# Kernel optimization log

Measured on AMD Instinct MI355X. Metric: run time of the kernel, lower is better.

The kernel has to match this reference:

```python
import jax, jax.numpy as jnp
import numpy as np

H, D, DIM = 8, 128, 1024   # heads, dim_head, model dim (inner_dim = H*D = DIM)
QB, N = 16, 512            # 'q' and 'n' dims of the [q, n, dim] inputs


def layer_norm(x, g, b, eps=1e-5):
    mu = x.mean(-1, keepdims=True)
    var = ((x - mu) ** 2).mean(-1, keepdims=True)
    return (x - mu) / jnp.sqrt(var + eps) * g + b


def setup_inputs() -> dict:
    key = jax.random.key(0)
    ks = jax.random.split(key, 8)
    rn = lambda k, shape, s=1.0: jax.random.normal(k, shape, jnp.float32) * s
    return {
        'q': rn(ks[0], (QB, N, DIM)),
        'k': rn(ks[1], (QB, N, DIM)),
        'v': rn(ks[2], (QB, N, DIM)),
        'ln_g': jnp.ones(DIM, jnp.float32),
        'ln_b': jnp.zeros(DIM, jnp.float32),
        'w_in': rn(ks[3], (H * D, DIM), 0.02),          # Linear(dim -> inner_dim), no bias
        'wp_w1': rn(ks[4], (D, 2 * D), 0.05),           # weight_predictor Linear(2d -> d)
        'wp_b1': jnp.zeros(D, jnp.float32),
        'wp_ln_g': jnp.ones(D, jnp.float32),
        'wp_ln_b': jnp.zeros(D, jnp.float32),
        'wp_w2': rn(ks[5], (3, D), 0.05),               # Linear(d -> 3)
        'wp_b2': jnp.zeros(3, jnp.float32),
        'w_out': rn(ks[6], (DIM, H * D), 0.02),         # output Linear(inner_dim -> dim)
        'b_out': jnp.zeros(DIM, jnp.float32),
    }


def reference(q, k, v, ln_g, ln_b, w_in, wp_w1, wp_b1, wp_ln_g, wp_ln_b,
              wp_w2, wp_b2, w_out, b_out):
    def proj(t):
        x = layer_norm(t, ln_g, ln_b) @ w_in.T                 # [Q, N, H*D]
        Qd, Nd = t.shape[0], t.shape[1]
        return x.reshape(Qd, Nd, H, D).transpose(2, 0, 1, 3)   # [h, q, n, d]

    f_q, f_k, f_v = proj(q), proj(k), proj(v)

    # cosine similarity component
    dots = jnp.einsum('hqnd,hqmd->hqnm', f_q, f_k)
    qn = jnp.linalg.norm(f_q, axis=-1)                          # [h, q, n]
    kn = jnp.linalg.norm(f_k, axis=-1)                          # [h, q, m]
    cosine_sim = dots / (qn[..., :, None] * kn[..., None, :])

    q_centered = f_q - f_q.mean(-1, keepdims=True)

    # variance component (unbiased variance, clipped ratio vs target_var=1)
    q_var = jnp.var(f_q, axis=-1, ddof=1)
    k_var = jnp.var(f_k, axis=-1, ddof=1)
    q_ratio = 2.0 * jnp.minimum(q_var, 1.0) / (q_var + 1.0)
    k_ratio = 2.0 * jnp.minimum(k_var, 1.0) / (k_var + 1.0)
    var_component = jnp.einsum('hqn,hqm->hqnm', q_ratio, k_ratio)

    # decorrelation-scaled covariance component (overwrites the dead loop in the source)
    q_flat = q_centered.reshape(H, -1, D)                        # [h, q*n, d]
    feat_corr = jnp.einsum('hnd,hne->hde', q_flat, q_flat) / q_flat.shape[1]
    feat_corr = feat_corr * (1.0 - jnp.eye(D, dtype=feat_corr.dtype))
    decorr_score = jnp.linalg.norm(feat_corr, axis=(-2, -1)) / (D * D)
    decorr_scale = jnp.exp(-5.0 * decorr_score)[:, None, None, None]
    cov_component = cosine_sim * decorr_scale

    # dynamic per-head weight mixing
    q_global = f_q.mean(axis=(1, 2))                             # [h, d]
    k_global = f_k.mean(axis=(1, 2))
    feats = jnp.concatenate([q_global, k_global], axis=-1)       # [h, 2d]
    h1 = jnp.maximum(layer_norm(feats @ wp_w1.T + wp_b1, wp_ln_g, wp_ln_b), 0.0)
    weights = jax.nn.softmax(h1 @ wp_w2.T + wp_b2, axis=-1)      # [h, 3]
    cw = weights[:, 0][:, None, None, None]
    vw = weights[:, 1][:, None, None, None]
    ww = weights[:, 2][:, None, None, None]
    mixed = cw * cosine_sim + vw * cov_component + ww * var_component

    out = jnp.einsum('hqnm,hqmd->hqnd', mixed, f_v)
    out = out.transpose(1, 2, 0, 3).reshape(q.shape[0], q.shape[1], H * D)
    return out @ w_out.T + b_out
```

## Files before the change

kernel.cpp:

```cpp
#include <hip/hip_runtime.h>
#include <hip/hip_bf16.h>

typedef unsigned short u16;
typedef __attribute__((ext_vector_type(8))) short short8;
typedef __attribute__((ext_vector_type(4))) float floatx4;

#define H 8
#define D 128
#define DIM 1024
#define QB 16
#define NSEQ 512
#define R 8192

__device__ inline u16 f2b(float x) {
    union { float f; unsigned int u; } c{x};
    unsigned int lsb = (c.u >> 16) & 1;
    unsigned int r = c.u + 0x7fffu + lsb;
    return (u16)(r >> 16);
}
__device__ inline float b2f(u16 u) {
    union { unsigned int i; float f; } c;
    c.i = (unsigned int)u << 16;
    return c.f;
}

#define GLOAD_LDS16(gptr, lptr)                                                        \
    __builtin_amdgcn_global_load_lds(                                                  \
        (const __attribute__((address_space(1))) unsigned int*)(gptr),                 \
        (__attribute__((address_space(3))) unsigned int*)(lptr), 16, 0, 0)

__global__ __launch_bounds__(256) void prep(const float* __restrict__ q,
                                            const float* __restrict__ k,
                                            const float* __restrict__ v,
                                            const float* __restrict__ g,
                                            const float* __restrict__ b,
                                            u16* __restrict__ out,
                                            const float* __restrict__ w_in,
                                            const float* __restrict__ w_out,
                                            u16* __restrict__ w_in16,
                                            u16* __restrict__ w_out16) {
    const int bb = blockIdx.x;
    const int tid = threadIdx.x;
    if (bb < 2048) {
        const int n4each = DIM * DIM / 4;
        int i = bb * 256 + tid;
        const float* src; u16* dst; int j;
        if (i < n4each) { src = w_in;  dst = w_in16;  j = i; }
        else            { src = w_out; dst = w_out16; j = i - n4each; }
        float4 vv = *(const float4*)(src + (size_t)j * 4);
        ushort4 pk;
        pk.x = f2b(vv.x); pk.y = f2b(vv.y); pk.z = f2b(vv.z); pk.w = f2b(vv.w);
        *(ushort4*)(dst + (size_t)j * 4) = pk;
        return;
    }
    const int b2 = bb - 2048;
    const int wv = tid >> 6, lane = tid & 63;
    const int row = b2 * 4 + wv;
    const int y = row >> 13, r = row & 8191;
    const float* src = (y == 0) ? q : (y == 1) ? k : v;
    const float* rp = src + (size_t)r * DIM;
    float4 x0 = *(const float4*)(rp + (0 * 64 + lane) * 4);
    float4 x1 = *(const float4*)(rp + (1 * 64 + lane) * 4);
    float4 x2 = *(const float4*)(rp + (2 * 64 + lane) * 4);
    float4 x3 = *(const float4*)(rp + (3 * 64 + lane) * 4);
    float sum = (x0.x + x0.y + x0.z + x0.w) + (x1.x + x1.y + x1.z + x1.w)
              + (x2.x + x2.y + x2.z + x2.w) + (x3.x + x3.y + x3.z + x3.w);
    float sq = x0.x*x0.x + x0.y*x0.y + x0.z*x0.z + x0.w*x0.w
             + x1.x*x1.x + x1.y*x1.y + x1.z*x1.z + x1.w*x1.w
             + x2.x*x2.x + x2.y*x2.y + x2.z*x2.z + x2.w*x2.w
             + x3.x*x3.x + x3.y*x3.y + x3.z*x3.z + x3.w*x3.w;
#pragma unroll
    for (int o = 32; o > 0; o >>= 1) {
        sum += __shfl_xor(sum, o);
        sq  += __shfl_xor(sq, o);
    }
    float mean = sum * (1.0f / DIM);
    float var = sq * (1.0f / DIM) - mean * mean;
    float rstd = rsqrtf(var + 1e-5f);
    u16* op = out + ((size_t)y * R + r) * DIM;
    float4 xs[4] = {x0, x1, x2, x3};
#pragma unroll
    for (int p = 0; p < 4; p++) {
        int e4 = (p * 64 + lane) * 4;
        float4 gv = *(const float4*)(g + e4);
        float4 bv = *(const float4*)(b + e4);
        ushort4 pk;
        pk.x = f2b((xs[p].x - mean) * rstd * gv.x + bv.x);
        pk.y = f2b((xs[p].y - mean) * rstd * gv.y + bv.y);
        pk.z = f2b((xs[p].z - mean) * rstd * gv.z + bv.z);
        pk.w = f2b((xs[p].w - mean) * rstd * gv.w + bv.w);
        *(ushort4*)(op + e4) = pk;
    }
}

__global__ __launch_bounds__(256) void gemm_qkv(const u16* __restrict__ A,
                                                const u16* __restrict__ B,
                                                u16* __restrict__ qT,
                                                u16* __restrict__ fqb,
                                                u16* __restrict__ kTh,
                                                u16* __restrict__ vT,
                                                float* __restrict__ qn,
                                                float* __restrict__ qm,
                                                float* __restrict__ qr,
                                                float* __restrict__ kn,
                                                float* __restrict__ kr) {
    __shared__ __align__(16) u16 smem[19712];
    u16* As  = smem;
    u16* Bs  = smem + 4096;
    u16* As2 = smem + 8192;
    u16* Bs2 = smem + 12288;
    float* sred = (float*)(smem + 18432);
    float* invb = (float*)(smem + 19456);

    const int tid = threadIdx.x;
    const int bb = blockIdx.x;
    const int xcd = bb & 7, j0 = bb >> 3;
    const int h = j0 & 7;
    const int rowblk = xcd * 24 + (j0 >> 3);
    const int m0 = rowblk * 128, n0 = h * 128;
    const int seg = rowblk >> 6;
    const int lrb = (rowblk & 63) * 128;

    const int wave = tid >> 6, lane = tid & 63;
    const int wm = (wave >> 1) * 64, wn = (wave & 1) * 64;
    const int fr = lane & 15, kq = lane >> 4;
    const int srow = tid >> 2, scol = (tid & 3) * 8;

    floatx4 acc[4][4] = {};
    const size_t aOff0 = (size_t)(m0 + srow) * DIM + scol;
    const size_t aOff1 = (size_t)(m0 + 64 + srow) * DIM + scol;
    const size_t bOff0 = (size_t)(n0 + srow) * DIM + scol;
    const size_t bOff1 = (size_t)(n0 + 64 + srow) * DIM + scol;

    for (int kt = 0; kt < DIM; kt += 64) {
        GLOAD_LDS16(A + aOff0 + kt, As + tid * 8);
        GLOAD_LDS16(A + aOff1 + kt, As + (256 + tid) * 8);
        GLOAD_LDS16(B + bOff0 + kt, Bs + tid * 8);
        GLOAD_LDS16(B + bOff1 + kt, Bs + (256 + tid) * 8);
        GLOAD_LDS16(A + aOff0 + kt + 32, As2 + tid * 8);
        GLOAD_LDS16(A + aOff1 + kt + 32, As2 + (256 + tid) * 8);
        GLOAD_LDS16(B + bOff0 + kt + 32, Bs2 + tid * 8);
        GLOAD_LDS16(B + bOff1 + kt + 32, Bs2 + (256 + tid) * 8);
        __syncthreads();
        short8 xf[4], wf[4];
#pragma unroll
        for (int i = 0; i < 4; i++)
            xf[i] = *(const short8*)&As[(wm + i * 16 + fr) * 32 + kq * 8];
#pragma unroll
        for (int j = 0; j < 4; j++)
            wf[j] = *(const short8*)&Bs[(wn + j * 16 + fr) * 32 + kq * 8];
#pragma unroll
        for (int j = 0; j < 4; j++)
#pragma unroll
            for (int i = 0; i < 4; i++)
                acc[j][i] = __builtin_amdgcn_mfma_f32_16x16x32_bf16(wf[j], xf[i], acc[j][i], 0, 0, 0);
        short8 xg[4], wg[4];
#pragma unroll
        for (int i = 0; i < 4; i++)
            xg[i] = *(const short8*)&As2[(wm + i * 16 + fr) * 32 + kq * 8];
#pragma unroll
        for (int j = 0; j < 4; j++)
            wg[j] = *(const short8*)&Bs2[(wn + j * 16 + fr) * 32 + kq * 8];
#pragma unroll
        for (int j = 0; j < 4; j++)
#pragma unroll
            for (int i = 0; i < 4; i++)
                acc[j][i] = __builtin_amdgcn_mfma_f32_16x16x32_bf16(wg[j], xg[i], acc[j][i], 0, 0, 0);
        __syncthreads();
    }

    if (seg <= 1) {
        const int half = wn >> 6;
#pragma unroll
        for (int i = 0; i < 4; i++) {
            float s = 0.0f, qs = 0.0f;
#pragma unroll
            for (int j = 0; j < 4; j++)
#pragma unroll
                for (int rg = 0; rg < 4; rg++) {
                    float vv = acc[j][i][rg];
                    s += vv; qs += vv * vv;
                }
            s += __shfl_xor(s, 16); qs += __shfl_xor(qs, 16);
            s += __shfl_xor(s, 32); qs += __shfl_xor(qs, 32);
            if (kq == 0) {
                int rl = wm + i * 16 + fr;
                sred[rl * 4 + half * 2 + 0] = s;
                sred[rl * 4 + half * 2 + 1] = qs;
            }
        }
        __syncthreads();
        if (tid < 128) {
            float sum = sred[tid * 4 + 0] + sred[tid * 4 + 2];
            float sq  = sred[tid * 4 + 1] + sred[tid * 4 + 3];
            float nrm = sqrtf(sq);
            float var = (sq - sum * sum * (1.0f / D)) * (1.0f / (D - 1));
            float ratio = 2.0f * fminf(var, 1.0f) / (var + 1.0f);
            size_t idx = (size_t)h * R + lrb + tid;
            if (seg == 0) {
                qn[idx] = nrm; qm[idx] = sum * (1.0f / D); qr[idx] = ratio;
            } else {
                kn[idx] = nrm; kr[idx] = ratio;
                invb[tid] = 1.0f / nrm;
            }
        }
        __syncthreads();
    }

    u16* dstT = (seg == 0) ? qT : (seg == 1) ? kTh : vT;
#pragma unroll
    for (int i = 0; i < 4; i++) {
        const int rl = wm + i * 16 + fr;
        const float sc = (seg == 1) ? invb[rl] : 1.0f;
#pragma unroll
        for (int j = 0; j < 4; j++) {
#pragma unroll
            for (int rg = 0; rg < 4; rg++) {
                const int cl = wn + j * 16 + kq * 4 + rg;
                dstT[(size_t)(h * D + cl) * R + lrb + rl] = f2b(acc[j][i][rg] * sc);
            }
        }
    }

    if (seg == 0) {
        __syncthreads();
        u16* Tw = smem + wave * 4608;
#pragma unroll
        for (int i = 0; i < 4; i++)
#pragma unroll
            for (int j = 0; j < 4; j++) {
                ushort4 pk;
                pk.x = f2b(acc[j][i][0]); pk.y = f2b(acc[j][i][1]);
                pk.z = f2b(acc[j][i][2]); pk.w = f2b(acc[j][i][3]);
                *(ushort4*)&Tw[(i * 16 + fr) * 72 + j * 16 + kq * 4] = pk;
            }
        __syncthreads();
#pragma unroll
        for (int p = 0; p < 16; p++) {
            int rloc = p * 4 + kq;
            int c4 = fr * 4;
            ushort4 v = *(const ushort4*)&Tw[rloc * 72 + c4];
            *(ushort4*)&fqb[(size_t)(lrb + wm + rloc) * DIM + h * D + wn + c4] = v;
        }
    }
}

__global__ __launch_bounds__(256) void fanout(const u16* __restrict__ qT,
                                              const u16* __restrict__ kTh,
                                              const u16* __restrict__ vT,
                                              const float* __restrict__ qm,
                                              const float* __restrict__ kn,
                                              const float* __restrict__ kr,
                                              float* __restrict__ qg,
                                              float* __restrict__ kg,
                                              float* __restrict__ ubuf,
                                              float* __restrict__ s2,
                                              float* __restrict__ P,
                                              u16* __restrict__ Mt,
                                              float* __restrict__ sv) {
    __shared__ __align__(16) u16 sm[17040];
    u16* As = sm;
    u16* Bs = sm + 8192;
    float* wbuf  = (float*)(sm + 16384);
    float* svred = (float*)(sm + 16512);
    float* redS  = (float*)(sm + 17024);

    const int bb = blockIdx.x;
    const int tid = threadIdx.x;
    const int wave = tid >> 6, lane = tid & 63;
    const int wm = (wave >> 1) * 64, wn = (wave & 1) * 64;
    const int fr = lane & 15, kq = lane >> 4;
    const int srow = tid >> 2, scol = (tid & 3) * 8;

    if (bb < 128) {
        const int qi = bb & 15, h = bb >> 4;
        const int m0g = qi * 512;
        const size_t a0 = (size_t)(h * D + srow) * R + m0g + scol;
        const size_t a1 = (size_t)(h * D + 64 + srow) * R + m0g + scol;
        const int e_id = tid & 127, mb16 = (tid >> 7) * 16;
        float svacc = 0.0f;
        floatx4 acc[4][4] = {};
        for (int kt = 0; kt < 512; kt += 64) {
#pragma unroll
            for (int kc = 0; kc < 2; kc++) {
                GLOAD_LDS16(vT + a0 + kt + kc * 32, As + kc * 4096 + tid * 8);
                GLOAD_LDS16(vT + a1 + kt + kc * 32, As + kc * 4096 + (256 + tid) * 8);
                GLOAD_LDS16(kTh + a0 + kt + kc * 32, Bs + kc * 4096 + tid * 8);
                GLOAD_LDS16(kTh + a1 + kt + kc * 32, Bs + kc * 4096 + (256 + tid) * 8);
            }
            if (tid < 64) wbuf[tid] = kr[(size_t)h * R + m0g + kt + tid];
            __syncthreads();
#pragma unroll
            for (int kc = 0; kc < 2; kc++) {
                short8 af[4], bf[4];
#pragma unroll
                for (int i = 0; i < 4; i++)
                    af[i] = *(const short8*)&As[kc * 4096 + (wm + i * 16 + fr) * 32 + kq * 8];
#pragma unroll
                for (int j = 0; j < 4; j++)
                    bf[j] = *(const short8*)&Bs[kc * 4096 + (wn + j * 16 + fr) * 32 + kq * 8];
#pragma unroll
                for (int i = 0; i < 4; i++)
#pragma unroll
                    for (int j = 0; j < 4; j++)
                        acc[i][j] = __builtin_amdgcn_mfma_f32_16x16x32_bf16(af[i], bf[j], acc[i][j], 0, 0, 0);
                short8 va = *(const short8*)&As[kc * 4096 + e_id * 32 + mb16];
                short8 vb = *(const short8*)&As[kc * 4096 + e_id * 32 + mb16 + 8];
#pragma unroll
                for (int jm = 0; jm < 8; jm++)
                    svacc += b2f((u16)va[jm]) * wbuf[kc * 32 + mb16 + jm];
#pragma unroll
                for (int jm = 0; jm < 8; jm++)
                    svacc += b2f((u16)vb[jm]) * wbuf[kc * 32 + mb16 + 8 + jm];
            }
            __syncthreads();
        }
        u16* mb = Mt + (size_t)(h * QB + qi) * D * D;
#pragma unroll
        for (int i = 0; i < 4; i++) {
            int er = wm + i * 16 + kq * 4;
#pragma unroll
            for (int j = 0; j < 4; j++) {
                int dc = wn + j * 16 + fr;
#pragma unroll
                for (int r = 0; r < 4; r++)
                    mb[(size_t)(er + r) * D + dc] = f2b(acc[i][j][r]);
            }
        }
        svred[tid] = svacc;
        __syncthreads();
        if (tid < 128)
            sv[(size_t)(h * QB + qi) * D + tid] = svred[tid] + svred[tid + 128];
    } else if (bb < 192) {
        const int t = bb - 128;
        const int c = t & 7, h = t >> 3;
        floatx4 acc[4][4] = {};
        const size_t a0 = (size_t)(h * D + srow) * R + c * 1024 + scol;
        const size_t a1 = (size_t)(h * D + 64 + srow) * R + c * 1024 + scol;
        for (int kt = 0; kt < 1024; kt += 64) {
#pragma unroll
            for (int kc = 0; kc < 2; kc++) {
                GLOAD_LDS16(qT + a0 + kt + kc * 32, As + kc * 4096 + tid * 8);
                GLOAD_LDS16(qT + a1 + kt + kc * 32, As + kc * 4096 + (256 + tid) * 8);
            }
            __syncthreads();
#pragma unroll
            for (int kc = 0; kc < 2; kc++) {
                short8 af[4], bf[4];
#pragma unroll
                for (int i = 0; i < 4; i++)
                    af[i] = *(const short8*)&As[kc * 4096 + (wm + i * 16 + fr) * 32 + kq * 8];
#pragma unroll
                for (int j = 0; j < 4; j++)
                    bf[j] = *(const short8*)&As[kc * 4096 + (wn + j * 16 + fr) * 32 + kq * 8];
#pragma unroll
                for (int i = 0; i < 4; i++)
#pragma unroll
                    for (int j = 0; j < 4; j++)
                        acc[i][j] = __builtin_amdgcn_mfma_f32_16x16x32_bf16(af[i], bf[j], acc[i][j], 0, 0, 0);
            }
            __syncthreads();
        }
        float* base = P + (size_t)(h * 8 + c) * (D * D);
#pragma unroll
        for (int i = 0; i < 4; i++) {
            int dr = wm + i * 16 + kq * 4;
#pragma unroll
            for (int j = 0; j < 4; j++) {
                int ec = wn + j * 16 + fr;
                float4 f4;
                f4.x = acc[i][j][0]; f4.y = acc[i][j][1];
                f4.z = acc[i][j][2]; f4.w = acc[i][j][3];
                *(float4*)&base[(size_t)ec * D + dr] = f4;
            }
        }
    } else {
        const int t = bb - 192;
        const int dg = t & 15, h = (t >> 4) & 7, mode = t >> 7;
        const u16* fT = mode ? kTh : qT;
        const float* wvec = mode ? kn : qm;
        const int wv = tid >> 6;
        float (*red)[4] = (float(*)[4])redS;
        const float* wp = wvec + (size_t)h * R;
        for (int dd = 0; dd < 8; dd++) {
            int d = dg * 8 + dd;
            const u16* rowp = fT + (size_t)(h * D + d) * R;
            float s = 0.0f, su = 0.0f;
            for (int it = 0; it < 8; it++) {
                int r = it * 1024 + tid * 4;
                uint2 pv = *(const uint2*)(rowp + r);
                float4 w = *(const float4*)(wp + r);
                float v0 = b2f((u16)(pv.x & 0xffffu)), v1 = b2f((u16)(pv.x >> 16));
                float v2 = b2f((u16)(pv.y & 0xffffu)), v3 = b2f((u16)(pv.y >> 16));
                if (mode) s += v0 * w.x + v1 * w.y + v2 * w.z + v3 * w.w;
                else {
                    s += v0 + v1 + v2 + v3;
                    su += v0 * w.x + v1 * w.y + v2 * w.z + v3 * w.w;
                }
            }
#pragma unroll
            for (int o = 32; o > 0; o >>= 1) {
                s += __shfl_xor(s, o);
                su += __shfl_xor(su, o);
            }
            if ((tid & 63) == 0) { red[0][wv] = s; red[1][wv] = su; }
            __syncthreads();
            if (tid == 0) {
                float S  = red[0][0] + red[0][1] + red[0][2] + red[0][3];
                float SU = red[1][0] + red[1][1] + red[1][2] + red[1][3];
                if (mode) kg[h * D + d] = S * (1.0f / R);
                else { qg[h * D + d] = S * (1.0f / R); ubuf[h * D + d] = SU; }
            }
            __syncthreads();
        }
        if (!mode && dg == 0) {
            float tt = 0.0f;
            for (int it = 0; it < 8; it++) {
                float4 m4 = *(const float4*)(qm + (size_t)h * R + it * 1024 + tid * 4);
                tt += m4.x * m4.x + m4.y * m4.y + m4.z * m4.z + m4.w * m4.w;
            }
#pragma unroll
            for (int o = 32; o > 0; o >>= 1) tt += __shfl_xor(tt, o);
            if ((tid & 63) == 0) red[0][wv] = tt;
            __syncthreads();
            if (tid == 0) s2[h] = red[0][0] + red[0][1] + red[0][2] + red[0][3];
        }
    }
}

__global__ __launch_bounds__(256) void decorr_sum(const float* __restrict__ P,
                                                  const float* __restrict__ ubuf,
                                                  const float* __restrict__ s2b,
                                                  float* __restrict__ Spart) {
    int bx = blockIdx.x, h = blockIdx.y, tid = threadIdx.x;
    float s2h = s2b[h];
    float S = 0.0f;
    for (int t = 0; t < 2; t++) {
        int de = bx * 512 + t * 256 + tid;
        int dd = de >> 7, ee = de & 127;
        float g = 0.0f;
        for (int c = 0; c < 8; c++)
            g += P[(size_t)(h * 8 + c) * (D * D) + de];
        if (dd != ee) {
            float vv = (g - ubuf[h * D + dd] - ubuf[h * D + ee] + s2h) * (1.0f / R);
            S += vv * vv;
        }
    }
#pragma unroll
    for (int o = 32; o > 0; o >>= 1) S += __shfl_xor(S, o);
    __shared__ float r1[4];
    if ((tid & 63) == 0) r1[tid >> 6] = S;
    __syncthreads();
    if (tid == 0) Spart[h * 32 + bx] = r1[0] + r1[1] + r1[2] + r1[3];
}

__global__ __launch_bounds__(256) void head_kernel(const float* __restrict__ Spart,
                                                   const float* __restrict__ qg,
                                                   const float* __restrict__ kg,
                                                   const float* __restrict__ w1,
                                                   const float* __restrict__ b1,
                                                   const float* __restrict__ lng,
                                                   const float* __restrict__ lnb,
                                                   const float* __restrict__ w2,
                                                   const float* __restrict__ b2,
                                                   float* __restrict__ coef) {
    int h = blockIdx.x, tid = threadIdx.x;
    __shared__ float s1[256], s2[256], s3[256];
    __shared__ float feats[256];
    float Ssum = 0.0f;
    for (int c = 0; c < 32; c++) Ssum += Spart[h * 32 + c];
    float dscale = expf(-5.0f * sqrtf(Ssum) / (float)(D * D));
    feats[tid] = (tid < 128) ? qg[h * D + tid] : kg[h * D + tid - 128];
    __syncthreads();
    float yv = 0.0f;
    if (tid < 128) {
        float a = b1[tid];
        for (int i = 0; i < 256; i++) a = fmaf(feats[i], w1[tid * 256 + i], a);
        yv = a;
    }
    s1[tid] = (tid < 128) ? yv : 0.0f;
    s2[tid] = (tid < 128) ? yv * yv : 0.0f;
    __syncthreads();
    for (int s = 128; s > 0; s >>= 1) {
        if (tid < s) { s1[tid] += s1[tid + s]; s2[tid] += s2[tid + s]; }
        __syncthreads();
    }
    float mean = s1[0] * (1.0f / 128.0f);
    float var = s2[0] * (1.0f / 128.0f) - mean * mean;
    float rstd = rsqrtf(var + 1e-5f);
    float rel = 0.0f;
    if (tid < 128)
        rel = fmaxf((yv - mean) * rstd * lng[tid] + lnb[tid], 0.0f);
    __syncthreads();
    s1[tid] = (tid < 128) ? rel * w2[0 * 128 + tid] : 0.0f;
    s2[tid] = (tid < 128) ? rel * w2[1 * 128 + tid] : 0.0f;
    s3[tid] = (tid < 128) ? rel * w2[2 * 128 + tid] : 0.0f;
    __syncthreads();
    for (int s = 128; s > 0; s >>= 1) {
        if (tid < s) { s1[tid] += s1[tid + s]; s2[tid] += s2[tid + s]; s3[tid] += s3[tid + s]; }
        __syncthreads();
    }
    if (tid == 0) {
        float g0 = s1[0] + b2[0], g1 = s2[0] + b2[1], g2 = s3[0] + b2[2];
        float mx = fmaxf(g0, fmaxf(g1, g2));
        float e0 = expf(g0 - mx), e1 = expf(g1 - mx), e2 = expf(g2 - mx);
        float inv = 1.0f / (e0 + e1 + e2);
        coef[h * 2 + 0] = e0 * inv + e1 * inv * dscale;
        coef[h * 2 + 1] = e2 * inv;
    }
}

__global__ __launch_bounds__(256) void attn_mfma(const u16* __restrict__ fqb,
                                                 const u16* __restrict__ Mt,
                                                 const float* __restrict__ qn,
                                                 const float* __restrict__ qr,
                                                 const float* __restrict__ sv,
                                                 const float* __restrict__ coef,
                                                 u16* __restrict__ outb) {
    __shared__ u16 As[128 * 128];
    __shared__ u16 Bs[128 * 128];
    const int nb = blockIdx.x, qi = blockIdx.y, h = blockIdx.z;
    const int tid = threadIdx.x;
    const int wave = tid >> 6, lane = tid & 63;
    const int wm = (wave >> 1) * 64, wn = (wave & 1) * 64;
    const int fr = lane & 15, kq = lane >> 4;
    const int srow = tid >> 2, scol = (tid & 3) * 8;
    const int n0g = qi * 512 + nb * 128;
    const size_t a0 = (size_t)(n0g + srow) * DIM + h * D + scol;
    const size_t a1 = (size_t)(n0g + 64 + srow) * DIM + h * D + scol;
    const u16* mtb = Mt + (size_t)(h * QB + qi) * D * D;
#pragma unroll
    for (int kc = 0; kc < 4; kc++) {
        GLOAD_LDS16(fqb + a0 + kc * 32, As + kc * 4096 + tid * 8);
        GLOAD_LDS16(fqb + a1 + kc * 32, As + kc * 4096 + (256 + tid) * 8);
        GLOAD_LDS16(mtb + (size_t)srow * D + kc * 32 + scol, Bs + kc * 4096 + tid * 8);
        GLOAD_LDS16(mtb + (size_t)(64 + srow) * D + kc * 32 + scol, Bs + kc * 4096 + (256 + tid) * 8);
    }
    __syncthreads();
    floatx4 acc[4][4] = {};
#pragma unroll
    for (int kc = 0; kc < 4; kc++) {
        short8 af[4], bf[4];
#pragma unroll
        for (int i = 0; i < 4; i++)
            af[i] = *(const short8*)&As[kc * 4096 + (wm + i * 16 + fr) * 32 + kq * 8];
#pragma unroll
        for (int j = 0; j < 4; j++)
            bf[j] = *(const short8*)&Bs[kc * 4096 + (wn + j * 16 + fr) * 32 + kq * 8];
#pragma unroll
        for (int i = 0; i < 4; i++)
#pragma unroll
            for (int j = 0; j < 4; j++)
                acc[i][j] = __builtin_amdgcn_mfma_f32_16x16x32_bf16(af[i], bf[j], acc[i][j], 0, 0, 0);
    }
    float c0 = coef[2 * h], c1 = coef[2 * h + 1];
#pragma unroll
    for (int i = 0; i < 4; i++) {
        int nr = n0g + wm + i * 16 + kq * 4;
        float4 nv = *(const float4*)&qn[(size_t)h * R + nr];
        float4 rv = *(const float4*)&qr[(size_t)h * R + nr];
        float sc1[4] = {c0 / nv.x, c0 / nv.y, c0 / nv.z, c0 / nv.w};
        float sc2[4] = {c1 * rv.x, c1 * rv.y, c1 * rv.z, c1 * rv.w};
#pragma unroll
        for (int j = 0; j < 4; j++) {
            int ec = wn + j * 16 + fr;
            float svv = sv[(size_t)(h * QB + qi) * D + ec];
#pragma unroll
            for (int r = 0; r < 4; r++)
                outb[(size_t)(nr + r) * DIM + h * D + ec] = f2b(sc1[r] * acc[i][j][r] + sc2[r] * svv);
        }
    }
}

__global__ __launch_bounds__(256) void gemm_out(const u16* __restrict__ A,
                                                const u16* __restrict__ B,
                                                const float* __restrict__ bias,
                                                float* __restrict__ C) {
    __shared__ u16 As[128 * 64];
    __shared__ u16 Bs[128 * 64];
    const int tid = threadIdx.x;
    const int bb = blockIdx.x;
    const int xcd = bb & 7, jj = bb >> 3;
    const int col = jj & 7, rowblk = xcd * 8 + (jj >> 3);
    const int m0 = rowblk * 128, n0 = col * 128;
    const int wave = tid >> 6, lane = tid & 63;
    const int wm = (wave >> 1) * 64, wn = (wave & 1) * 64;
    const int fr = lane & 15, kq = lane >> 4;
    const int srow = tid >> 2, scol = (tid & 3) * 8;
    floatx4 acc[4][4] = {};
    const size_t aOff0 = (size_t)(m0 + srow) * DIM + scol;
    const size_t aOff1 = (size_t)(m0 + 64 + srow) * DIM + scol;
    const size_t bOff0 = (size_t)(n0 + srow) * DIM + scol;
    const size_t bOff1 = (size_t)(n0 + 64 + srow) * DIM + scol;
    for (int kt = 0; kt < DIM; kt += 64) {
        GLOAD_LDS16(A + aOff0 + kt, As + tid * 8);
        GLOAD_LDS16(A + aOff1 + kt, As + (256 + tid) * 8);
        GLOAD_LDS16(A + aOff0 + kt + 32, As + (512 + tid) * 8);
        GLOAD_LDS16(A + aOff1 + kt + 32, As + (768 + tid) * 8);
        GLOAD_LDS16(B + bOff0 + kt, Bs + tid * 8);
        GLOAD_LDS16(B + bOff1 + kt, Bs + (256 + tid) * 8);
        GLOAD_LDS16(B + bOff0 + kt + 32, Bs + (512 + tid) * 8);
        GLOAD_LDS16(B + bOff1 + kt + 32, Bs + (768 + tid) * 8);
        __syncthreads();
        short8 af[4], bf[4];
#pragma unroll
        for (int i = 0; i < 4; i++)
            af[i] = *(const short8*)&As[(wm + i * 16 + fr) * 32 + kq * 8];
#pragma unroll
        for (int j = 0; j < 4; j++)
            bf[j] = *(const short8*)&Bs[(wn + j * 16 + fr) * 32 + kq * 8];
#pragma unroll
        for (int i = 0; i < 4; i++)
#pragma unroll
            for (int j = 0; j < 4; j++)
                acc[i][j] = __builtin_amdgcn_mfma_f32_16x16x32_bf16(af[i], bf[j], acc[i][j], 0, 0, 0);
        short8 ag[4], bg[4];
#pragma unroll
        for (int i = 0; i < 4; i++)
            ag[i] = *(const short8*)&As[4096 + (wm + i * 16 + fr) * 32 + kq * 8];
#pragma unroll
        for (int j = 0; j < 4; j++)
            bg[j] = *(const short8*)&Bs[4096 + (wn + j * 16 + fr) * 32 + kq * 8];
#pragma unroll
        for (int i = 0; i < 4; i++)
#pragma unroll
            for (int j = 0; j < 4; j++)
                acc[i][j] = __builtin_amdgcn_mfma_f32_16x16x32_bf16(ag[i], bg[j], acc[i][j], 0, 0, 0);
        __syncthreads();
    }
#pragma unroll
    for (int i = 0; i < 4; i++) {
        int rbase = m0 + wm + i * 16 + kq * 4;
#pragma unroll
        for (int j = 0; j < 4; j++) {
            int c = n0 + wn + j * 16 + fr;
            float badd = bias[c];
#pragma unroll
            for (int r = 0; r < 4; r++)
                C[(size_t)(rbase + r) * DIM + c] = acc[i][j][r] + badd;
        }
    }
}

extern "C" void kernel_launch(void* const* d_in, const int* in_sizes, int n_in,
                              void* d_out, int out_size, void* d_ws, size_t ws_size,
                              hipStream_t stream) {
    (void)in_sizes; (void)n_in; (void)out_size; (void)ws_size;
    const float* q      = (const float*)d_in[0];
    const float* k      = (const float*)d_in[1];
    const float* v      = (const float*)d_in[2];
    const float* ln_g   = (const float*)d_in[3];
    const float* ln_b   = (const float*)d_in[4];
    const float* w_in   = (const float*)d_in[5];
    const float* wp_w1  = (const float*)d_in[6];
    const float* wp_b1  = (const float*)d_in[7];
    const float* wp_lng = (const float*)d_in[8];
    const float* wp_lnb = (const float*)d_in[9];
    const float* wp_w2  = (const float*)d_in[10];
    const float* wp_b2  = (const float*)d_in[11];
    const float* w_out  = (const float*)d_in[12];
    const float* b_out  = (const float*)d_in[13];
    float* out = (float*)d_out;

    constexpr size_t F = (size_t)R * DIM;
    u16* lnall   = (u16*)d_ws;
    u16* fqb     = lnall + 3 * F;
    u16* qT      = fqb + F;
    u16* kTh     = qT + F;
    u16* vT      = kTh + F;
    u16* w_in16  = vT + F;
    u16* w_out16 = w_in16 + (size_t)DIM * DIM;
    u16* Mt      = w_out16 + (size_t)DIM * DIM;
    float* P     = (float*)(Mt + (size_t)H * QB * D * D);
    float* qn    = P + (size_t)32 * H * D * D;
    float* qm    = qn + (size_t)H * R;
    float* qr    = qm + (size_t)H * R;
    float* kn    = qr + (size_t)H * R;
    float* kr    = kn + (size_t)H * R;
    float* qg    = kr + (size_t)H * R;
    float* kg    = qg + H * D;
    float* ubuf  = kg + H * D;
    float* s2    = ubuf + H * D;
    float* Spart = s2 + H;
    float* coef  = Spart + H * 8;
    float* svb   = coef + 16;
    float* SpartN = qm;

    prep<<<8192, 256, 0, stream>>>(q, k, v, ln_g, ln_b, lnall,
                                   w_in, w_out, w_in16, w_out16);

    gemm_qkv<<<1536, 256, 0, stream>>>(lnall, w_in16, qT, fqb, kTh, vT,
                                       qn, qm, qr, kn, kr);

    fanout<<<448, 256, 0, stream>>>(qT, kTh, vT, qm, kn, kr,
                                    qg, kg, ubuf, s2, P, Mt, svb);

    decorr_sum<<<dim3(32, H), 256, 0, stream>>>(P, ubuf, s2, SpartN);

    head_kernel<<<H, 256, 0, stream>>>(SpartN, qg, kg, wp_w1, wp_b1,
                                       wp_lng, wp_lnb, wp_w2, wp_b2, coef);

    attn_mfma<<<dim3(4, QB, H), 256, 0, stream>>>(fqb, Mt, qn, qr, svb, coef, lnall);

    gemm_out<<<512, 256, 0, stream>>>(lnall, w_out16, b_out, out);
}
```

Baseline: 314.0 us.

## Fuse decorrelation reduction and head-weight MLP into attention kernel

Removes the separate decorr_sum and head_kernel launches. Each attention block now recomputes the per-head decorrelation norm and the weight-predictor MLP itself, overlapped with its async LDS loads. This saves two kernel launches and their serialization. In exchange, every block redundantly reads the full per-head P partials and w1, which greatly multiplies memory traffic.

```diff
diff --git a/kernel.cpp b/kernel.cpp
--- a/kernel.cpp
+++ b/kernel.cpp
@@ -428,97 +428,26 @@
     }
 }
 
-__global__ __launch_bounds__(256) void decorr_sum(const float* __restrict__ P,
-                                                  const float* __restrict__ ubuf,
-                                                  const float* __restrict__ s2b,
-                                                  float* __restrict__ Spart) {
-    int bx = blockIdx.x, h = blockIdx.y, tid = threadIdx.x;
-    float s2h = s2b[h];
-    float S = 0.0f;
-    for (int t = 0; t < 2; t++) {
-        int de = bx * 512 + t * 256 + tid;
-        int dd = de >> 7, ee = de & 127;
-        float g = 0.0f;
-        for (int c = 0; c < 8; c++)
-            g += P[(size_t)(h * 8 + c) * (D * D) + de];
-        if (dd != ee) {
-            float vv = (g - ubuf[h * D + dd] - ubuf[h * D + ee] + s2h) * (1.0f / R);
-            S += vv * vv;
-        }
-    }
-#pragma unroll
-    for (int o = 32; o > 0; o >>= 1) S += __shfl_xor(S, o);
-    __shared__ float r1[4];
-    if ((tid & 63) == 0) r1[tid >> 6] = S;
-    __syncthreads();
-    if (tid == 0) Spart[h * 32 + bx] = r1[0] + r1[1] + r1[2] + r1[3];
-}
-
-__global__ __launch_bounds__(256) void head_kernel(const float* __restrict__ Spart,
-                                                   const float* __restrict__ qg,
-                                                   const float* __restrict__ kg,
-                                                   const float* __restrict__ w1,
-                                                   const float* __restrict__ b1,
-                                                   const float* __restrict__ lng,
-                                                   const float* __restrict__ lnb,
-                                                   const float* __restrict__ w2,
-                                                   const float* __restrict__ b2,
-                                                   float* __restrict__ coef) {
-    int h = blockIdx.x, tid = threadIdx.x;
-    __shared__ float s1[256], s2[256], s3[256];
-    __shared__ float feats[256];
-    float Ssum = 0.0f;
-    for (int c = 0; c < 32; c++) Ssum += Spart[h * 32 + c];
-    float dscale = expf(-5.0f * sqrtf(Ssum) / (float)(D * D));
-    feats[tid] = (tid < 128) ? qg[h * D + tid] : kg[h * D + tid - 128];
-    __syncthreads();
-    float yv = 0.0f;
-    if (tid < 128) {
-        float a = b1[tid];
-        for (int i = 0; i < 256; i++) a = fmaf(feats[i], w1[tid * 256 + i], a);
-        yv = a;
-    }
-    s1[tid] = (tid < 128) ? yv : 0.0f;
-    s2[tid] = (tid < 128) ? yv * yv : 0.0f;
-    __syncthreads();
-    for (int s = 128; s > 0; s >>= 1) {
-        if (tid < s) { s1[tid] += s1[tid + s]; s2[tid] += s2[tid + s]; }
-        __syncthreads();
-    }
-    float mean = s1[0] * (1.0f / 128.0f);
-    float var = s2[0] * (1.0f / 128.0f) - mean * mean;
-    float rstd = rsqrtf(var + 1e-5f);
-    float rel = 0.0f;
-    if (tid < 128)
-        rel = fmaxf((yv - mean) * rstd * lng[tid] + lnb[tid], 0.0f);
-    __syncthreads();
-    s1[tid] = (tid < 128) ? rel * w2[0 * 128 + tid] : 0.0f;
-    s2[tid] = (tid < 128) ? rel * w2[1 * 128 + tid] : 0.0f;
-    s3[tid] = (tid < 128) ? rel * w2[2 * 128 + tid] : 0.0f;
-    __syncthreads();
-    for (int s = 128; s > 0; s >>= 1) {
-        if (tid < s) { s1[tid] += s1[tid + s]; s2[tid] += s2[tid + s]; s3[tid] += s3[tid + s]; }
-        __syncthreads();
-    }
-    if (tid == 0) {
-        float g0 = s1[0] + b2[0], g1 = s2[0] + b2[1], g2 = s3[0] + b2[2];
-        float mx = fmaxf(g0, fmaxf(g1, g2));
-        float e0 = expf(g0 - mx), e1 = expf(g1 - mx), e2 = expf(g2 - mx);
-        float inv = 1.0f / (e0 + e1 + e2);
-        coef[h * 2 + 0] = e0 * inv + e1 * inv * dscale;
-        coef[h * 2 + 1] = e2 * inv;
-    }
-}
-
-__global__ __launch_bounds__(256) void attn_mfma(const u16* __restrict__ fqb,
-                                                 const u16* __restrict__ Mt,
-                                                 const float* __restrict__ qn,
-                                                 const float* __restrict__ qr,
-                                                 const float* __restrict__ sv,
-                                                 const float* __restrict__ coef,
-                                                 u16* __restrict__ outb) {
+__global__ __launch_bounds__(256) void attn2(const u16* __restrict__ fqb,
+                                             const u16* __restrict__ Mt,
+                                             const float* __restrict__ qn,
+                                             const float* __restrict__ qr,
+                                             const float* __restrict__ sv,
+                                             const float* __restrict__ P,
+                                             const float* __restrict__ ubuf,
+                                             const float* __restrict__ s2b,
+                                             const float* __restrict__ qg,
+                                             const float* __restrict__ kg,
+                                             const float* __restrict__ w1,
+                                             const float* __restrict__ b1,
+                                             const float* __restrict__ lng,
+                                             const float* __restrict__ lnb,
+                                             const float* __restrict__ w2,
+                                             const float* __restrict__ b2,
+                                             u16* __restrict__ outb) {
     __shared__ u16 As[128 * 128];
     __shared__ u16 Bs[128 * 128];
+    __shared__ float hscratch[1024];
     const int nb = blockIdx.x, qi = blockIdx.y, h = blockIdx.z;
     const int tid = threadIdx.x;
     const int wave = tid >> 6, lane = tid & 63;
@@ -529,6 +458,7 @@
     const size_t a0 = (size_t)(n0g + srow) * DIM + h * D + scol;
     const size_t a1 = (size_t)(n0g + 64 + srow) * DIM + h * D + scol;
     const u16* mtb = Mt + (size_t)(h * QB + qi) * D * D;
+
 #pragma unroll
     for (int kc = 0; kc < 4; kc++) {
         GLOAD_LDS16(fqb + a0 + kc * 32, As + kc * 4096 + tid * 8);
@@ -536,7 +466,80 @@
         GLOAD_LDS16(mtb + (size_t)srow * D + kc * 32 + scol, Bs + kc * 4096 + tid * 8);
         GLOAD_LDS16(mtb + (size_t)(64 + srow) * D + kc * 32 + scol, Bs + kc * 4096 + (256 + tid) * 8);
     }
+
+    float c0, c1;
+    {
+        float s2h = s2b[h];
+        float part = 0.0f;
+        for (int k = 0; k < 64; k++) {
+            int de = k * 256 + tid;
+            int dd = de >> 7, ee = de & 127;
+            float gsum = 0.0f;
+#pragma unroll
+            for (int c = 0; c < 8; c++)
+                gsum += P[(size_t)(h * 8 + c) * (D * D) + de];
+            if (dd != ee) {
+                float vv = (gsum - ubuf[h * D + dd] - ubuf[h * D + ee] + s2h) * (1.0f / R);
+                part += vv * vv;
+            }
+        }
+#pragma unroll
+        for (int o = 32; o > 0; o >>= 1) part += __shfl_xor(part, o);
+        if (lane == 0) hscratch[wave] = part;
+        __syncthreads();
+        float Ssum = hscratch[0] + hscratch[1] + hscratch[2] + hscratch[3];
+        float dscale = expf(-5.0f * sqrtf(Ssum) / (float)(D * D));
+        __syncthreads();
+
+        float* hs1 = hscratch;
+        float* hs2 = hscratch + 256;
+        float* hs3 = hscratch + 512;
+        float* hfe = hscratch + 768;
+        hfe[tid] = (tid < 128) ? qg[h * D + tid] : kg[h * D + tid - 128];
+        __syncthreads();
+        float yv = 0.0f;
+        if (tid < 128) {
+            float a = b1[tid];
+            for (int i = 0; i < 256; i++) a = fmaf(hfe[i], w1[tid * 256 + i], a);
+            yv = a;
+        }
+        hs1[tid] = (tid < 128) ? yv : 0.0f;
+        hs2[tid] = (tid < 128) ? yv * yv : 0.0f;
+        __syncthreads();
+        for (int s = 128; s > 0; s >>= 1) {
+            if (tid < s) { hs1[tid] += hs1[tid + s]; hs2[tid] += hs2[tid + s]; }
+            __syncthreads();
+        }
+        float mean = hs1[0] * (1.0f / 128.0f);
+        float var = hs2[0] * (1.0f / 128.0f) - mean * mean;
+        float rstd = rsqrtf(var + 1e-5f);
+        float rel = 0.0f;
+        if (tid < 128)
+            rel = fmaxf((yv - mean) * rstd * lng[tid] + lnb[tid], 0.0f);
+        __syncthreads();
+        hs1[tid] = (tid < 128) ? rel * w2[0 * 128 + tid] : 0.0f;
+        hs2[tid] = (tid < 128) ? rel * w2[1 * 128 + tid] : 0.0f;
+        hs3[tid] = (tid < 128) ? rel * w2[2 * 128 + tid] : 0.0f;
+        __syncthreads();
+        for (int s = 128; s > 0; s >>= 1) {
+            if (tid < s) { hs1[tid] += hs1[tid + s]; hs2[tid] += hs2[tid + s]; hs3[tid] += hs3[tid + s]; }
+            __syncthreads();
+        }
+        if (tid == 0) {
+            float g0 = hs1[0] + b2[0], g1 = hs2[0] + b2[1], g2 = hs3[0] + b2[2];
+            float mx = fmaxf(g0, fmaxf(g1, g2));
+            float e0 = expf(g0 - mx), e1 = expf(g1 - mx), e2 = expf(g2 - mx);
+            float inv = 1.0f / (e0 + e1 + e2);
+            hs1[0] = e0 * inv + e1 * inv * dscale;
+            hs1[1] = e2 * inv;
+        }
+        __syncthreads();
+        c0 = hs1[0]; c1 = hs1[1];
+    }
+
+    asm volatile("s_waitcnt vmcnt(0)" ::: "memory");
     __syncthreads();
+
     floatx4 acc[4][4] = {};
 #pragma unroll
     for (int kc = 0; kc < 4; kc++) {
@@ -553,7 +556,6 @@
             for (int j = 0; j < 4; j++)
                 acc[i][j] = __builtin_amdgcn_mfma_f32_16x16x32_bf16(af[i], bf[j], acc[i][j], 0, 0, 0);
     }
-    float c0 = coef[2 * h], c1 = coef[2 * h + 1];
 #pragma unroll
     for (int i = 0; i < 4; i++) {
         int nr = n0g + wm + i * 16 + kq * 4;
@@ -684,7 +686,6 @@
     float* Spart = s2 + H;
     float* coef  = Spart + H * 8;
     float* svb   = coef + 16;
-    float* SpartN = qm;
 
     prep<<<8192, 256, 0, stream>>>(q, k, v, ln_g, ln_b, lnall,
                                    w_in, w_out, w_in16, w_out16);
@@ -695,12 +696,10 @@
     fanout<<<448, 256, 0, stream>>>(qT, kTh, vT, qm, kn, kr,
                                     qg, kg, ubuf, s2, P, Mt, svb);
 
-    decorr_sum<<<dim3(32, H), 256, 0, stream>>>(P, ubuf, s2, SpartN);
-
-    head_kernel<<<H, 256, 0, stream>>>(SpartN, qg, kg, wp_w1, wp_b1,
-                                       wp_lng, wp_lnb, wp_w2, wp_b2, coef);
-
-    attn_mfma<<<dim3(4, QB, H), 256, 0, stream>>>(fqb, Mt, qn, qr, svb, coef, lnall);
+    attn2<<<dim3(4, QB, H), 256, 0, stream>>>(fqb, Mt, qn, qr, svb,
+                                              P, ubuf, s2, qg, kg,
+                                              wp_w1, wp_b1, wp_lng, wp_lnb,
+                                              wp_w2, wp_b2, lnall);
 
     gemm_out<<<512, 256, 0, stream>>>(lnall, w_out16, b_out, out);
 }
```

Result: slower. 333.8 us (+6.3%).

## Fuse global q/k mean statistics into the QKV GEMM epilogue with atomics

Applied to the files above, without the earlier changes.

The per-head column sums (qg, kg), the mean-weighted sums (ubuf) and the sum of squared row means (s2) are now reduced in the gemm_qkv epilogue from the accumulator registers. They are combined across blocks with atomicAdd into buffers that extra prep blocks zero first. This drops the 256 fanout blocks that re-read the transposed q/k feature maps from global memory, and removes the qm buffer. It also splits decorr_sum over 64 blocks per head instead of 32, and moves the 1/R mean scaling into head_kernel. The cost is a heavier GEMM epilogue with extra shared-memory reductions, syncs and float atomics, whose ordering is nondeterministic.

```diff
diff --git a/kernel.cpp b/kernel.cpp
--- a/kernel.cpp
+++ b/kernel.cpp
@@ -38,9 +38,15 @@
                                             const float* __restrict__ w_in,
                                             const float* __restrict__ w_out,
                                             u16* __restrict__ w_in16,
-                                            u16* __restrict__ w_out16) {
+                                            u16* __restrict__ w_out16,
+                                            float* __restrict__ zbuf) {
     const int bb = blockIdx.x;
     const int tid = threadIdx.x;
+    if (bb >= 8192) {
+        int idx = (bb - 8192) * 256 + tid;
+        if (idx < 3 * H * D + H) zbuf[idx] = 0.0f;
+        return;
+    }
     if (bb < 2048) {
         const int n4each = DIM * DIM / 4;
         int i = bb * 256 + tid;
@@ -100,10 +106,13 @@
                                                 u16* __restrict__ kTh,
                                                 u16* __restrict__ vT,
                                                 float* __restrict__ qn,
-                                                float* __restrict__ qm,
                                                 float* __restrict__ qr,
                                                 float* __restrict__ kn,
-                                                float* __restrict__ kr) {
+                                                float* __restrict__ kr,
+                                                float* __restrict__ qg,
+                                                float* __restrict__ kg,
+                                                float* __restrict__ ubuf,
+                                                float* __restrict__ s2g) {
     __shared__ __align__(16) u16 smem[19712];
     u16* As  = smem;
     u16* Bs  = smem + 4096;
@@ -198,11 +207,69 @@
             float ratio = 2.0f * fminf(var, 1.0f) / (var + 1.0f);
             size_t idx = (size_t)h * R + lrb + tid;
             if (seg == 0) {
-                qn[idx] = nrm; qm[idx] = sum * (1.0f / D); qr[idx] = ratio;
+                qn[idx] = nrm; qr[idx] = ratio;
             } else {
                 kn[idx] = nrm; kr[idx] = ratio;
                 invb[tid] = 1.0f / nrm;
             }
+        }
+        __syncthreads();
+
+        float* colg = (float*)(smem + 8192);
+        float* colu = (float*)(smem + 8704);
+        for (int j = 0; j < 4; j++) {
+            float cg[4] = {0, 0, 0, 0};
+            float cu[4] = {0, 0, 0, 0};
+#pragma unroll
+            for (int i = 0; i < 4; i++) {
+                int rl = wm + i * 16 + fr;
+                float qmv = (sred[rl * 4 + 0] + sred[rl * 4 + 2]) * (1.0f / D);
+#pragma unroll
+                for (int rg = 0; rg < 4; rg++) {
+                    float vv = acc[j][i][rg];
+                    cg[rg] += vv;
+                    cu[rg] += qmv * vv;
+                }
+            }
+#pragma unroll
+            for (int o = 1; o < 16; o <<= 1) {
+#pragma unroll
+                for (int rg = 0; rg < 4; rg++) {
+                    cg[rg] += __shfl_xor(cg[rg], o);
+                    cu[rg] += __shfl_xor(cu[rg], o);
+                }
+            }
+            if (fr == 0) {
+#pragma unroll
+                for (int rg = 0; rg < 4; rg++) {
+                    int c = wn + j * 16 + kq * 4 + rg;
+                    colg[c * 2 + (wm >> 6)] = cg[rg];
+                    colu[c * 2 + (wm >> 6)] = cu[rg];
+                }
+            }
+        }
+        __syncthreads();
+        if (tid < 128) {
+            float vg = colg[tid * 2] + colg[tid * 2 + 1];
+            if (seg == 0) {
+                atomicAdd(&qg[h * D + tid], vg);
+                atomicAdd(&ubuf[h * D + tid], colu[tid * 2] + colu[tid * 2 + 1]);
+            } else {
+                atomicAdd(&kg[h * D + tid], vg);
+            }
+        }
+        if (seg == 0) {
+            float q2 = 0.0f;
+            if (tid < 128) {
+                float qmv = (sred[tid * 4 + 0] + sred[tid * 4 + 2]) * (1.0f / D);
+                q2 = qmv * qmv;
+            }
+#pragma unroll
+            for (int o = 32; o > 0; o >>= 1) q2 += __shfl_xor(q2, o);
+            if ((tid & 63) == 0) invb[tid >> 6] = q2;
+            __syncthreads();
+            if (tid == 0)
+                atomicAdd(&s2g[h], invb[0] + invb[1] + invb[2] + invb[3]);
         }
         __syncthreads();
     }
@@ -248,13 +315,7 @@
 __global__ __launch_bounds__(256) void fanout(const u16* __restrict__ qT,
                                               const u16* __restrict__ kTh,
                                               const u16* __restrict__ vT,
-                                              const float* __restrict__ qm,
-                                              const float* __restrict__ kn,
                                               const float* __restrict__ kr,
-                                              float* __restrict__ qg,
-                                              float* __restrict__ kg,
-                                              float* __restrict__ ubuf,
-                                              float* __restrict__ s2,
                                               float* __restrict__ P,
                                               u16* __restrict__ Mt,
                                               float* __restrict__ sv) {
@@ -263,7 +324,6 @@
     u16* Bs = sm + 8192;
     float* wbuf  = (float*)(sm + 16384);
     float* svred = (float*)(sm + 16512);
-    float* redS  = (float*)(sm + 17024);
 
     const int bb = blockIdx.x;
     const int tid = threadIdx.x;
@@ -331,7 +391,7 @@
         __syncthreads();
         if (tid < 128)
             sv[(size_t)(h * QB + qi) * D + tid] = svred[tid] + svred[tid + 128];
-    } else if (bb < 192) {
+    } else {
         const int t = bb - 128;
         const int c = t & 7, h = t >> 3;
         floatx4 acc[4][4] = {};
@@ -374,57 +434,6 @@
                 *(float4*)&base[(size_t)ec * D + dr] = f4;
             }
         }
-    } else {
-        const int t = bb - 192;
-        const int dg = t & 15, h = (t >> 4) & 7, mode = t >> 7;
-        const u16* fT = mode ? kTh : qT;
-        const float* wvec = mode ? kn : qm;
-        const int wv = tid >> 6;
-        float (*red)[4] = (float(*)[4])redS;
-        const float* wp = wvec + (size_t)h * R;
-        for (int dd = 0; dd < 8; dd++) {
-            int d = dg * 8 + dd;
-            const u16* rowp = fT + (size_t)(h * D + d) * R;
-            float s = 0.0f, su = 0.0f;
-            for (int it = 0; it < 8; it++) {
-                int r = it * 1024 + tid * 4;
-                uint2 pv = *(const uint2*)(rowp + r);
-                float4 w = *(const float4*)(wp + r);
-                float v0 = b2f((u16)(pv.x & 0xffffu)), v1 = b2f((u16)(pv.x >> 16));
-                float v2 = b2f((u16)(pv.y & 0xffffu)), v3 = b2f((u16)(pv.y >> 16));
-                if (mode) s += v0 * w.x + v1 * w.y + v2 * w.z + v3 * w.w;
-                else {
-                    s += v0 + v1 + v2 + v3;
-                    su += v0 * w.x + v1 * w.y + v2 * w.z + v3 * w.w;
-                }
-            }
-#pragma unroll
-            for (int o = 32; o > 0; o >>= 1) {
-                s += __shfl_xor(s, o);
-                su += __shfl_xor(su, o);
-            }
-            if ((tid & 63) == 0) { red[0][wv] = s; red[1][wv] = su; }
-            __syncthreads();
-            if (tid == 0) {
-                float S  = red[0][0] + red[0][1] + red[0][2] + red[0][3];
-                float SU = red[1][0] + red[1][1] + red[1][2] + red[1][3];
-                if (mode) kg[h * D + d] = S * (1.0f / R);
-                else { qg[h * D + d] = S * (1.0f / R); ubuf[h * D + d] = SU; }
-            }
-            __syncthreads();
-        }
-        if (!mode && dg == 0) {
-            float tt = 0.0f;
-            for (int it = 0; it < 8; it++) {
-                float4 m4 = *(const float4*)(qm + (size_t)h * R + it * 1024 + tid * 4);
-                tt += m4.x * m4.x + m4.y * m4.y + m4.z * m4.z + m4.w * m4.w;
-            }
-#pragma unroll
-            for (int o = 32; o > 0; o >>= 1) tt += __shfl_xor(tt, o);
-            if ((tid & 63) == 0) red[0][wv] = tt;
-            __syncthreads();
-            if (tid == 0) s2[h] = red[0][0] + red[0][1] + red[0][2] + red[0][3];
-        }
     }
 }
 
@@ -434,24 +443,23 @@
                                                   float* __restrict__ Spart) {
     int bx = blockIdx.x, h = blockIdx.y, tid = threadIdx.x;
     float s2h = s2b[h];
+    int de = bx * 256 + tid;
+    int dd = de >> 7, ee = de & 127;
+    float g = 0.0f;
+#pragma unroll
+    for (int c = 0; c < 8; c++)
+        g += P[(size_t)(h * 8 + c) * (D * D) + de];
     float S = 0.0f;
-    for (int t = 0; t < 2; t++) {
-        int de = bx * 512 + t * 256 + tid;
-        int dd = de >> 7, ee = de & 127;
-        float g = 0.0f;
-        for (int c = 0; c < 8; c++)
-            g += P[(size_t)(h * 8 + c) * (D * D) + de];
-        if (dd != ee) {
-            float vv = (g - ubuf[h * D + dd] - ubuf[h * D + ee] + s2h) * (1.0f / R);
-            S += vv * vv;
-        }
+    if (dd != ee) {
+        float vv = (g - ubuf[h * D + dd] - ubuf[h * D + ee] + s2h) * (1.0f / R);
+        S = vv * vv;
     }
 #pragma unroll
     for (int o = 32; o > 0; o >>= 1) S += __shfl_xor(S, o);
     __shared__ float r1[4];
     if ((tid & 63) == 0) r1[tid >> 6] = S;
     __syncthreads();
-    if (tid == 0) Spart[h * 32 + bx] = r1[0] + r1[1] + r1[2] + r1[3];
+    if (tid == 0) Spart[h * 64 + bx] = r1[0] + r1[1] + r1[2] + r1[3];
 }
 
 __global__ __launch_bounds__(256) void head_kernel(const float* __restrict__ Spart,
@@ -468,9 +476,9 @@
     __shared__ float s1[256], s2[256], s3[256];
     __shared__ float feats[256];
     float Ssum = 0.0f;
-    for (int c = 0; c < 32; c++) Ssum += Spart[h * 32 + c];
+    for (int c = 0; c < 64; c++) Ssum += Spart[h * 64 + c];
     float dscale = expf(-5.0f * sqrtf(Ssum) / (float)(D * D));
-    feats[tid] = (tid < 128) ? qg[h * D + tid] : kg[h * D + tid - 128];
+    feats[tid] = ((tid < 128) ? qg[h * D + tid] : kg[h * D + tid - 128]) * (1.0f / R);
     __syncthreads();
     float yv = 0.0f;
     if (tid < 128) {
@@ -686,16 +694,15 @@
     float* svb   = coef + 16;
     float* SpartN = qm;
 
-    prep<<<8192, 256, 0, stream>>>(q, k, v, ln_g, ln_b, lnall,
-                                   w_in, w_out, w_in16, w_out16);
+    prep<<<8205, 256, 0, stream>>>(q, k, v, ln_g, ln_b, lnall,
+                                   w_in, w_out, w_in16, w_out16, qg);
 
     gemm_qkv<<<1536, 256, 0, stream>>>(lnall, w_in16, qT, fqb, kTh, vT,
-                                       qn, qm, qr, kn, kr);
-
-    fanout<<<448, 256, 0, stream>>>(qT, kTh, vT, qm, kn, kr,
-                                    qg, kg, ubuf, s2, P, Mt, svb);
-
-    decorr_sum<<<dim3(32, H), 256, 0, stream>>>(P, ubuf, s2, SpartN);
+                                       qn, qr, kn, kr, qg, kg, ubuf, s2);
+
+    fanout<<<192, 256, 0, stream>>>(qT, kTh, vT, kr, P, Mt, svb);
+
+    decorr_sum<<<dim3(64, H), 256, 0, stream>>>(P, ubuf, s2, SpartN);
 
     head_kernel<<<H, 256, 0, stream>>>(SpartN, qg, kg, wp_w1, wp_b1,
                                        wp_lng, wp_lnb, wp_w2, wp_b2, coef);
```

Result: no change. 313.5 us (-0.1%).
